# Kernel optimization log

Hardware: AMD Instinct MI355X
Metric: run time of the kernel (lower is better)

The kernel has to match this reference:

```python
import jax, jax.numpy as jnp
import numpy as np

N_ITEMS = 30000
N_HOPS = 2
TMP = 0.2
EPS = 1e-12


def _l2norm(x):
    # F.normalize(x, dim=1): x / max(||x||_2, eps)
    n = jnp.sqrt(jnp.sum(x * x, axis=1, keepdims=True))
    return x / jnp.maximum(n, EPS)


def setup_inputs() -> dict:
    key = jax.random.key(0)
    ks = jax.random.split(key, 12)
    n_users, n_entities, n_items, d = 50000, 100000, N_ITEMS, 64
    n_rel, n_fac, n_cls = 16, 4, 8
    n_edges, n_inter = 1000000, 500000
    return {
        'user_emb': jax.random.normal(ks[0], (n_users, d), jnp.float32),
        'entity_emb': jax.random.normal(ks[1], (n_entities, d), jnp.float32),
        'cls_emb': jax.random.normal(ks[2], (n_cls, d), jnp.float32),
        'latent_emb': jax.random.normal(ks[3], (n_fac, d), jnp.float32),
        'relation_emb': jax.random.normal(ks[4], (n_rel, d), jnp.float32),
        'disen_weight_att': jax.random.normal(ks[5], (n_fac, n_rel), jnp.float32),
        'edge_index': jax.random.randint(ks[6], (2, n_edges), 0, n_entities, jnp.int32),
        'edge_type': jax.random.randint(ks[7], (n_edges,), 0, n_rel, jnp.int32),
        'inter_user': jax.random.randint(ks[8], (n_inter,), 0, n_users, jnp.int32),
        'inter_item': jax.random.randint(ks[9], (n_inter,), 0, n_items, jnp.int32),
        'inter_val': jax.random.uniform(ks[10], (n_inter,), jnp.float32),
        'inter_cls': jax.random.randint(ks[11], (n_inter,), 0, n_cls, jnp.int32),
    }


def _cls_aggregate(entity_emb, user_emb, cls_emb, latent_emb, relation_emb,
                   disen_weight_att, edge_index, edge_type,
                   inter_user, inter_item, inter_val, inter_cls,
                   n_users, n_cls):
    n_entities = entity_emb.shape[0]
    item_emb = entity_emb[:N_ITEMS]
    # --- KG aggregate: scatter_mean over head of entity_emb[tail]*rel[edge_type]
    head, tail = edge_index[0], edge_index[1]
    msg = entity_emb[tail] * relation_emb[edge_type]            # [E, d]
    ent_sum = jax.ops.segment_sum(msg, head, num_segments=n_entities)
    cnt = jax.ops.segment_sum(jnp.ones_like(head, jnp.float32), head,
                              num_segments=n_entities)
    entity_agg = ent_sum / jnp.maximum(cnt, 1.0)[:, None]
    # --- user aggregate: sparse interact_mat @ item_emb
    u_msg = inter_val[:, None] * item_emb[inter_item]           # [I, d]
    user_agg = jax.ops.segment_sum(u_msg, inter_user, num_segments=n_users)
    # --- intent attention
    user_disen_att = jax.nn.softmax(user_emb @ latent_emb.T, axis=1)  # [U, F]
    disen_weight = jax.nn.softmax(disen_weight_att, axis=-1) @ relation_emb  # [F, d]
    user_agg = user_disen_att @ disen_weight + user_agg
    # --- class attention: inter_cls_mat[c] @ item_emb for each class
    user_cls_att = jax.nn.softmax(user_emb @ cls_emb.T, axis=1)  # [U, C]
    seg = inter_cls * n_users + inter_user
    user_cls = jax.ops.segment_sum(u_msg, seg, num_segments=n_cls * n_users)
    user_cls = user_cls.reshape(n_cls, n_users, -1)              # [C, U, d]
    user_agg = jnp.einsum('cud,uc->ud', user_cls, user_cls_att) + user_agg
    return entity_agg, user_agg


def _mutual_information(t, temperature):
    nt = _l2norm(t)
    scores = jnp.exp(nt @ nt.T / temperature)
    return -jnp.sum(jnp.log(jnp.diag(scores) / jnp.sum(scores, axis=1)))


def reference(user_emb, entity_emb, cls_emb, latent_emb, relation_emb,
              disen_weight_att, edge_index, edge_type, inter_user,
              inter_item, inter_val, inter_cls):
    n_users = user_emb.shape[0]
    n_cls = cls_emb.shape[0]
    entity_res, user_res = entity_emb, user_emb
    e, u = entity_emb, user_emb
    for _ in range(N_HOPS):
        e, u = _cls_aggregate(e, u, cls_emb, latent_emb, relation_emb,
                              disen_weight_att, edge_index, edge_type,
                              inter_user, inter_item, inter_val, inter_cls,
                              n_users, n_cls)
        e = _l2norm(e)
        u = _l2norm(u)
        entity_res = entity_res + e
        user_res = user_res + u
    cor_loss = _mutual_information(disen_weight_att, TMP)
    return entity_res, user_res, cor_loss
```

## Files before the change

kernel.cpp:

```cpp
#include <hip/hip_runtime.h>
#include <math.h>

typedef unsigned int uint;

constexpr int N_USERS  = 50000;
constexpr int N_ENT    = 100000;
constexpr int D        = 64;
constexpr int N_FAC    = 4;
constexpr int N_CLS    = 8;
constexpr int N_REL    = 16;
constexpr int N_EDGES  = 1000000;
constexpr int N_INTER  = 500000;

constexpr int BSH      = 7;
constexpr int SPB      = 1 << BSH;
constexpr int NBKT_E   = (N_ENT   + SPB - 1) / SPB;
constexpr int NBKT_U   = (N_USERS + SPB - 1) / SPB;
constexpr int CHUNK    = 4096;
constexpr int NB_E     = (N_EDGES + CHUNK - 1) / CHUNK;
constexpr int NB_U     = (N_INTER + CHUNK - 1) / CHUNK;
constexpr int EBUF_CAP = 3072;

constexpr int E_ROWS   = N_ENT + 1;

constexpr int CVT_BLKS = 2047;

static_assert(NB_E <= 256 && NB_U <= 256, "k_final local scan assumes NB <= 256");

typedef _Float16 h2_t __attribute__((ext_vector_type(2)));
union U32H2 { uint u; h2_t h; };

__device__ inline float h_lo(uint v) { U32H2 x; x.u = v; return (float)x.h.x; }
__device__ inline float h_hi(uint v) { U32H2 x; x.u = v; return (float)x.h.y; }
__device__ inline uint packh(float a, float b) {
    auto r = __builtin_amdgcn_cvt_pkrtz(a, b);
    union { decltype(r) h; uint u; } x;
    x.h = r;
    return x.u;
}

__device__ inline int wscan64_incl(int x, int lane) {
#pragma unroll
    for (int off = 1; off < 64; off <<= 1) {
        int v = __shfl_up(x, off, 64);
        if (lane >= off) x += v;
    }
    return x;
}

__device__ inline int block_scan_incl(int x, int* wsum) {
    int lane = threadIdx.x & 63, wv = threadIdx.x >> 6;
#pragma unroll
    for (int off = 1; off < 64; off <<= 1) {
        int v = __shfl_up(x, off, 64);
        if (lane >= off) x += v;
    }
    if (lane == 63) wsum[wv] = x;
    __syncthreads();
    if (wv == 0 && lane < 16) {
        int s = wsum[lane];
#pragma unroll
        for (int off = 1; off < 16; off <<= 1) {
            int v = __shfl_up(s, off, 64);
            if (lane >= off) s += v;
        }
        wsum[lane] = s;
    }
    __syncthreads();
    if (wv > 0) x += wsum[wv - 1];
    return x;
}

__global__ void k_cvt_dw(const float2* __restrict__ in, uint* __restrict__ out,
                         int n_src, int n_out,
                         const float* __restrict__ datt,
                         const float* __restrict__ rel,
                         float* __restrict__ dw,
                         float* __restrict__ loss_out,
                         uint4* __restrict__ relh4,
                         int* __restrict__ totE,
                         int* __restrict__ totU) {
    __shared__ float p[N_FAC][N_REL];
    __shared__ float nrm[N_FAC];
    __shared__ float sc[N_FAC][N_FAC];
    int t = threadIdx.x;
    int b = blockIdx.x;
    if (b < CVT_BLKS) {
        for (int i = b * 256 + t; i < n_out; i += CVT_BLKS * 256) {
            if (i < n_src) {
                float2 v = in[i];
                out[i] = packh(v.x, v.y);
            } else {
                out[i] = 0u;
            }
        }
        return;
    }
    for (int s = t; s < NBKT_E; s += 256) totE[s] = 0;
    for (int s = t; s < NBKT_U; s += 256) totU[s] = 0;
    for (int s = t; s < N_REL * 8; s += 256) {
        int r = s >> 3, kk = s & 7;
        const float* rp = rel + r * 64 + kk * 8;
        relh4[s] = make_uint4(packh(rp[0], rp[1]), packh(rp[2], rp[3]),
                              packh(rp[4], rp[5]), packh(rp[6], rp[7]));
    }
    if (t < N_FAC) {
        float m = -1e30f;
        for (int r = 0; r < N_REL; ++r) m = fmaxf(m, datt[t * N_REL + r]);
        float tmp[N_REL]; float s = 0.f;
        for (int r = 0; r < N_REL; ++r) { tmp[r] = expf(datt[t * N_REL + r] - m); s += tmp[r]; }
        for (int r = 0; r < N_REL; ++r) p[t][r] = tmp[r] / s;
        float ss = 0.f;
        for (int r = 0; r < N_REL; ++r) { float v = datt[t * N_REL + r]; ss += v * v; }
        nrm[t] = fmaxf(sqrtf(ss), 1e-12f);
    }
    __syncthreads();
    if (t < D) {
        for (int f = 0; f < N_FAC; ++f) {
            float acc = 0.f;
            for (int r = 0; r < N_REL; ++r) acc += p[f][r] * rel[r * D + t];
            dw[f * D + t] = acc;
        }
    }
    if (t < N_FAC * N_FAC) {
        int i = t >> 2, j = t & 3;
        float s = 0.f;
        for (int r = 0; r < N_REL; ++r) s += datt[i * N_REL + r] * datt[j * N_REL + r];
        s /= nrm[i] * nrm[j];
        sc[i][j] = expf(s * 5.0f);
    }
    __syncthreads();
    if (t == 0) {
        float loss = 0.f;
        for (int i = 0; i < N_FAC; ++i) {
            float rowsum = 0.f;
            for (int j = 0; j < N_FAC; ++j) rowsum += sc[i][j];
            loss += logf(sc[i][i] / rowsum);
        }
        *loss_out = -loss;
    }
}

__global__ void k_sort(const int* __restrict__ headE, const int* __restrict__ tailE,
                       const int* __restrict__ etype,
                       const int* __restrict__ iu, const int* __restrict__ ii,
                       const int* __restrict__ icls, const float* __restrict__ ival,
                       uint2* __restrict__ stagE, int* __restrict__ GE, int* __restrict__ RE,
                       uint2* __restrict__ stagU, int* __restrict__ GU, int* __restrict__ RU,
                       int* __restrict__ totE, int* __restrict__ totU) {
    __shared__ int hist[NBKT_E];
    __shared__ int soff[NBKT_E + 1];
    __shared__ int cursor[NBKT_E];
    __shared__ int wsum[16];
    __shared__ uint2 sorted[CHUNK];
    int bid = blockIdx.x;
    bool isE = bid < NB_E;
    int blk  = isE ? bid : bid - NB_E;
    int n    = isE ? N_EDGES : N_INTER;
    int nbkt = isE ? NBKT_E : NBKT_U;
    int base = blk * CHUNK;
    int end  = min(base + CHUNK, n);
    int cblk = end - base;

    for (int b = threadIdx.x; b < nbkt; b += 256) hist[b] = 0;
    __syncthreads();

    uint2 ent[16]; int ebk[16];
#pragma unroll
    for (int j = 0; j < 16; ++j) {
        int i = base + threadIdx.x + j * 256;
        ebk[j] = -1;
        if (i < end) {
            uint x, y; int b;
            if (isE) {
                int h = headE[i];
                x = (uint)h; y = (uint)((tailE[i] << 4) | etype[i]); b = h >> BSH;
            } else {
                int u = iu[i];
                x = (uint)((u << 15) | ii[i]);
                y = (__float_as_uint(ival[i]) & ~7u) | (uint)icls[i];
                b = u >> BSH;
            }
            ent[j] = make_uint2(x, y); ebk[j] = b;
            atomicAdd(&hist[b], 1);
        }
    }
    __syncthreads();

    int b0 = threadIdx.x * 4;
    int lsum[4]; int mysum = 0;
#pragma unroll
    for (int j = 0; j < 4; ++j) {
        int b = b0 + j;
        int v = (b < nbkt) ? hist[b] : 0;
        lsum[j] = mysum; mysum += v;
    }
    int excl = block_scan_incl(mysum, wsum) - mysum;
#pragma unroll
    for (int j = 0; j < 4; ++j) {
        int b = b0 + j;
        if (b < nbkt) soff[b] = excl + lsum[j];
    }
    if (threadIdx.x == 0) soff[nbkt] = cblk;
    __syncthreads();
    for (int b = threadIdx.x; b < nbkt; b += 256) cursor[b] = soff[b];
    __syncthreads();

#pragma unroll
    for (int j = 0; j < 16; ++j) {
        if (ebk[j] >= 0) {
            int p = atomicAdd(&cursor[ebk[j]], 1);
            sorted[p] = ent[j];
        }
    }
    __syncthreads();

    uint2* stag = isE ? stagE : stagU;
    int* G = isE ? GE : GU;
    int* R = isE ? RE : RU;
    int* tot = isE ? totE : totU;
    for (int i = threadIdx.x; i < cblk; i += 256) stag[blk * CHUNK + i] = sorted[i];
    for (int b = threadIdx.x; b < nbkt; b += 256) {
        G[blk * nbkt + b] = hist[b];
        if (hist[b]) atomicAdd(&tot[b], hist[b]);
    }
    for (int b = threadIdx.x; b <= nbkt; b += 256) R[blk * (nbkt + 1) + b] = soff[b];
}

__device__ inline void scan_tot(const int* __restrict__ tot, int* __restrict__ base,
                                int nbkt, int l, int* __restrict__ off_last, int nseg) {
    int carry = 0;
    for (int b = 0; b < nbkt; b += 64) {
        int x = (b + l < nbkt) ? tot[b + l] : 0;
        int incl = wscan64_incl(x, l);
        if (b + l < nbkt) base[b + l] = carry + incl - x;
        carry += __shfl(incl, 63, 64);
    }
    if (l == 0) {
        base[nbkt] = carry;
        off_last[nseg] = carry;
        off_last[nseg + 1] = carry;
    }
}

__global__ void k_base(const int* __restrict__ totE, int* __restrict__ baseE,
                       const int* __restrict__ totU, int* __restrict__ baseU,
                       int* __restrict__ eoff, int* __restrict__ uoff) {
    int t = threadIdx.x;
    if (t < 64) scan_tot(totE, baseE, NBKT_E, t, eoff, N_ENT);
    else        scan_tot(totU, baseU, NBKT_U, t - 64, uoff, N_USERS);
}

__global__ void k_final(const uint2* __restrict__ stagE, const int* __restrict__ GE,
                        const int* __restrict__ RE, const int* __restrict__ baseE,
                        const uint2* __restrict__ stagU, const int* __restrict__ GU,
                        const int* __restrict__ RU, const int* __restrict__ baseU,
                        int* __restrict__ eoff, int* __restrict__ uoff,
                        int* __restrict__ epay, int2* __restrict__ ipv) {
    __shared__ uint2 ebuf[EBUF_CAP];
    __shared__ int cnt[SPB], soff[SPB], cur[SPB];
    __shared__ int wsum[16];
    int bid = blockIdx.x;
    bool isE = bid < NBKT_E;
    int bkt = bid < NBKT_E ? bid : bid - NBKT_E;
    const uint2* stag = isE ? stagE : stagU;
    const int* G  = isE ? GE : GU;
    const int* R  = isE ? RE : RU;
    const int* bb = isE ? baseE : baseU;
    int* off      = isE ? eoff : uoff;
    int NB   = isE ? NB_E : NB_U;
    int nbkt = isE ? NBKT_E : NBKT_U;
    int nseg = isE ? N_ENT : N_USERS;
    int r0 = bb[bkt], r1 = bb[bkt + 1];
    int bsz = r1 - r0;
    int t = threadIdx.x;
    int myc = (t < NB) ? G[t * nbkt + bkt] : 0;
    int mydst = block_scan_incl(myc, wsum) - myc;
    if (t < SPB) cnt[t] = 0;
    if (t < NB) {
        int rs  = R[t * (nbkt + 1) + bkt];
        int re  = R[t * (nbkt + 1) + bkt + 1];
        for (int j = rs; j < re; ++j) {
            int d = mydst + (j - rs);
            if (d < EBUF_CAP) ebuf[d] = stag[t * CHUNK + j];
        }
    }
    __syncthreads();
    for (int i = t; i < bsz; i += 256) {
        uint2 e = ebuf[i];
        int s = (int)(isE ? e.x : (e.x >> 15)) & (SPB - 1);
        atomicAdd(&cnt[s], 1);
    }
    __syncthreads();
    if (t < 64) {
        int a0 = cnt[2 * t], a1 = cnt[2 * t + 1];
        int incl = wscan64_incl(a0 + a1, t);
        int excl = incl - (a0 + a1);
        soff[2 * t] = excl;
        soff[2 * t + 1] = excl + a0;
    }
    __syncthreads();
    if (t < SPB) {
        cur[t] = soff[t];
        int seg = bkt * SPB + t;
        if (seg < nseg) off[seg] = r0 + soff[t];
    }
    __syncthreads();
    for (int i = t; i < bsz; i += 256) {
        uint2 e = ebuf[i];
        int s = (int)(isE ? e.x : (e.x >> 15)) & (SPB - 1);
        int pos = r0 + atomicAdd(&cur[s], 1);
        if (isE) {
            epay[pos] = (int)e.y;
        } else {
            int item = (int)(e.x & 0x7FFF), cls = (int)(e.y & 7u);
            ipv[pos] = make_int2((item << 3) | cls, (int)(e.y & ~7u));
        }
    }
}

template<int MODE>
__global__ __launch_bounds__(256)
void k_hop(const uint4* __restrict__ etab,
           const float4* __restrict__ entbase,
           const float4* __restrict__ usrbase,
           const uint4* __restrict__ ustate_in,
           const uint4* __restrict__ relh4,
           const int* __restrict__ eoff,
           const int* __restrict__ epay,
           const int* __restrict__ uoff,
           const int2* __restrict__ ipv,
           const float4* __restrict__ latent4,
           const float4* __restrict__ cls4,
           const float4* __restrict__ dw4,
           float* __restrict__ att4,
           float* __restrict__ att8,
           uint4* __restrict__ stateE_out,
           uint4* __restrict__ stateU_out,
           float4* __restrict__ outE,
           float4* __restrict__ outU) {
    __shared__ uint4  s_rel[N_REL * 8];
    __shared__ float4 s_dw [N_FAC * 16];
    __shared__ float4 s_lat[N_FAC * 16];
    __shared__ float4 s_cls[N_CLS * 16];
    {
        int t = threadIdx.x;
        if (t < N_REL * 8) s_rel[t] = relh4[t];
        if (t < N_FAC * 16) s_dw[t] = dw4[t];
        if (MODE == 0) {
            if (t < N_FAC * 16) s_lat[t] = latent4[t];
            if (t < N_CLS * 16) s_cls[t] = cls4[t];
        }
    }
    __syncthreads();

    int gid = blockIdx.x * 256 + threadIdx.x;
    int gw = gid >> 3;
    int k = threadIdx.x & 7;
    if (gw >= E_ROWS + N_USERS) return;
    bool isEnt = gw < E_ROWS;
    float a0 = 0.f, a1 = 0.f, a2 = 0.f, a3 = 0.f;
    float a4 = 0.f, a5 = 0.f, a6 = 0.f, a7 = 0.f;

    if (isEnt) {
        int w = gw;
        int beg = eoff[w], end = eoff[w + 1];
        int nE = end - beg;
        const int* pp = epay + beg;
        int pc[8];
#pragma unroll
        for (int q = 0; q < 8; ++q) pc[q] = pp[q];
        for (int bse = 0; bse < nE; bse += 8) {
            int c = nE - bse;
            int pn[8];
#pragma unroll
            for (int q = 0; q < 8; ++q) pn[q] = pp[bse + 8 + q];
            uint4 ev[8], rl[8];
#pragma unroll
            for (int q = 0; q < 8; ++q) {
                int p = (q < c) ? pc[q] : (N_ENT << 4);
                ev[q] = etab[(((size_t)(p >> 4)) << 3) + k];
                rl[q] = s_rel[((p & 15) << 3) + k];
            }
#pragma unroll
            for (int q = 0; q < 8; ++q) {
                a0 = fmaf(h_lo(ev[q].x), h_lo(rl[q].x), a0);
                a1 = fmaf(h_hi(ev[q].x), h_hi(rl[q].x), a1);
                a2 = fmaf(h_lo(ev[q].y), h_lo(rl[q].y), a2);
                a3 = fmaf(h_hi(ev[q].y), h_hi(rl[q].y), a3);
                a4 = fmaf(h_lo(ev[q].z), h_lo(rl[q].z), a4);
                a5 = fmaf(h_hi(ev[q].z), h_hi(rl[q].z), a5);
                a6 = fmaf(h_lo(ev[q].w), h_lo(rl[q].w), a6);
                a7 = fmaf(h_hi(ev[q].w), h_hi(rl[q].w), a7);
            }
#pragma unroll
            for (int q = 0; q < 8; ++q) pc[q] = pn[q];
        }
        float ss = a0*a0 + a1*a1 + a2*a2 + a3*a3 + a4*a4 + a5*a5 + a6*a6 + a7*a7;
#pragma unroll
        for (int m = 1; m < 8; m <<= 1) ss += __shfl_xor(ss, m, 8);
        float s = 1.0f / fmaxf(sqrtf(ss), 1e-12f);
        float v0 = a0*s, v1 = a1*s, v2 = a2*s, v3 = a3*s;
        float v4 = a4*s, v5 = a5*s, v6 = a6*s, v7 = a7*s;
        if (MODE == 0) {
            stateE_out[((size_t)w << 3) + k] =
                make_uint4(packh(v0, v1), packh(v2, v3), packh(v4, v5), packh(v6, v7));
        } else if (w < N_ENT) {
            size_t b = ((size_t)w << 4) + (k << 1);
            float4 b0 = entbase[b], b1 = entbase[b + 1];
            uint4 own = etab[((size_t)w << 3) + k];
            float4 o0 = make_float4(b0.x + h_lo(own.x) + v0, b0.y + h_hi(own.x) + v1,
                                    b0.z + h_lo(own.y) + v2, b0.w + h_hi(own.y) + v3);
            float4 o1 = make_float4(b1.x + h_lo(own.z) + v4, b1.y + h_hi(own.z) + v5,
                                    b1.z + h_lo(own.w) + v6, b1.w + h_hi(own.w) + v7);
            outE[b] = o0; outE[b + 1] = o1;
        }
    } else {
        int w = gw - E_ROWS;
        int beg = uoff[w], end = uoff[w + 1];
        int nE = end - beg;
        const int2* pv = ipv + beg;

        float af0, af1, af2, af3, a8v;
        if (MODE == 0) {
            size_t bb = ((size_t)w << 4) + (k << 1);
            float4 x0 = usrbase[bb], x1 = usrbase[bb + 1];
            float d[12];
#pragma unroll
            for (int f = 0; f < 12; ++f) {
                const float4* lp = (f < 4 ? s_lat + f * 16 : s_cls + (f - 4) * 16) + (k << 1);
                float4 l0 = lp[0], l1 = lp[1];
                d[f] = x0.x*l0.x + x0.y*l0.y + x0.z*l0.z + x0.w*l0.w
                     + x1.x*l1.x + x1.y*l1.y + x1.z*l1.z + x1.w*l1.w;
            }
#pragma unroll
            for (int j = 0; j < 12; ++j) {
#pragma unroll
                for (int off = 1; off < 8; off <<= 1) d[j] += __shfl_xor(d[j], off, 8);
            }
            float m4 = fmaxf(fmaxf(d[0], d[1]), fmaxf(d[2], d[3]));
            float e40 = expf(d[0] - m4), e41 = expf(d[1] - m4);
            float e42 = expf(d[2] - m4), e43 = expf(d[3] - m4);
            float r4 = 1.0f / (e40 + e41 + e42 + e43);
            af0 = e40 * r4; af1 = e41 * r4; af2 = e42 * r4; af3 = e43 * r4;
            float m8 = d[4];
#pragma unroll
            for (int c = 1; c < 8; ++c) m8 = fmaxf(m8, d[4 + c]);
            float e8[8]; float s8 = 0.f;
#pragma unroll
            for (int c = 0; c < 8; ++c) { e8[c] = expf(d[4 + c] - m8); s8 += e8[c]; }
            float a8e = e8[0];
#pragma unroll
            for (int c = 1; c < 8; ++c) if (k == c) a8e = e8[c];
            a8v = a8e / s8;
        } else {
            af0 = att4[w * 4 + 0]; af1 = att4[w * 4 + 1];
            af2 = att4[w * 4 + 2]; af3 = att4[w * 4 + 3];
            a8v = att8[w * 8 + k];
        }

        int2 ec[8];
#pragma unroll
        for (int q = 0; q < 8; ++q) ec[q] = pv[q];
        for (int bse = 0; bse < nE; bse += 8) {
            int c = nE - bse;
            int2 en[8];
#pragma unroll
            for (int q = 0; q < 8; ++q) en[q] = pv[bse + 8 + q];
            uint4 ev[8]; float wg[8];
#pragma unroll
            for (int q = 0; q < 8; ++q) {
                int p = ec[q].x;
                int pe = (q < c) ? p : 0;
                ev[q] = etab[(((size_t)(pe >> 3)) << 3) + k];
                float wgt = __int_as_float(ec[q].y) * (1.0f + __shfl(a8v, p & 7, 8));
                wg[q] = (q < c) ? wgt : 0.0f;
            }
#pragma unroll
            for (int q = 0; q < 8; ++q) {
                a0 = fmaf(h_lo(ev[q].x), wg[q], a0);
                a1 = fmaf(h_hi(ev[q].x), wg[q], a1);
                a2 = fmaf(h_lo(ev[q].y), wg[q], a2);
                a3 = fmaf(h_hi(ev[q].y), wg[q], a3);
                a4 = fmaf(h_lo(ev[q].z), wg[q], a4);
                a5 = fmaf(h_hi(ev[q].z), wg[q], a5);
                a6 = fmaf(h_lo(ev[q].w), wg[q], a6);
                a7 = fmaf(h_hi(ev[q].w), wg[q], a7);
            }
#pragma unroll
            for (int q = 0; q < 8; ++q) ec[q] = en[q];
        }
        {
            const float4* dd0 = s_dw + 0 * 16 + (k << 1);
            const float4* dd1 = s_dw + 1 * 16 + (k << 1);
            const float4* dd2 = s_dw + 2 * 16 + (k << 1);
            const float4* dd3 = s_dw + 3 * 16 + (k << 1);
#pragma unroll
            for (int f = 0; f < 4; ++f) {
                float a = (f == 0) ? af0 : (f == 1) ? af1 : (f == 2) ? af2 : af3;
                const float4* dd = (f == 0) ? dd0 : (f == 1) ? dd1 : (f == 2) ? dd2 : dd3;
                float4 d0 = dd[0], d1 = dd[1];
                a0 = fmaf(a, d0.x, a0); a1 = fmaf(a, d0.y, a1);
                a2 = fmaf(a, d0.z, a2); a3 = fmaf(a, d0.w, a3);
                a4 = fmaf(a, d1.x, a4); a5 = fmaf(a, d1.y, a5);
                a6 = fmaf(a, d1.z, a6); a7 = fmaf(a, d1.w, a7);
            }
        }
        float ss = a0*a0 + a1*a1 + a2*a2 + a3*a3 + a4*a4 + a5*a5 + a6*a6 + a7*a7;
#pragma unroll
        for (int m = 1; m < 8; m <<= 1) ss += __shfl_xor(ss, m, 8);
        float s = 1.0f / fmaxf(sqrtf(ss), 1e-12f);
        float v0 = a0*s, v1 = a1*s, v2 = a2*s, v3 = a3*s;
        float v4 = a4*s, v5 = a5*s, v6 = a6*s, v7 = a7*s;
        if (MODE == 0) {
            stateU_out[((size_t)w << 3) + k] =
                make_uint4(packh(v0, v1), packh(v2, v3), packh(v4, v5), packh(v6, v7));
            float d[12];
#pragma unroll
            for (int f = 0; f < 12; ++f) {
                const float4* lp = (f < 4 ? s_lat + f * 16 : s_cls + (f - 4) * 16) + (k << 1);
                float4 l0 = lp[0], l1 = lp[1];
                d[f] = v0*l0.x + v1*l0.y + v2*l0.z + v3*l0.w
                     + v4*l1.x + v5*l1.y + v6*l1.z + v7*l1.w;
            }
#pragma unroll
            for (int j = 0; j < 12; ++j) {
#pragma unroll
                for (int off = 1; off < 8; off <<= 1) d[j] += __shfl_xor(d[j], off, 8);
            }
            float m4 = fmaxf(fmaxf(d[0], d[1]), fmaxf(d[2], d[3]));
            float e40 = expf(d[0] - m4), e41 = expf(d[1] - m4);
            float e42 = expf(d[2] - m4), e43 = expf(d[3] - m4);
            float r4 = 1.0f / (e40 + e41 + e42 + e43);
            if (k < 4) {
                float v = (k == 0) ? e40 : (k == 1) ? e41 : (k == 2) ? e42 : e43;
                att4[w * 4 + k] = v * r4;
            }
            float m8 = d[4];
#pragma unroll
            for (int c = 1; c < 8; ++c) m8 = fmaxf(m8, d[4 + c]);
            float e8[8]; float s8 = 0.f;
#pragma unroll
            for (int c = 0; c < 8; ++c) { e8[c] = expf(d[4 + c] - m8); s8 += e8[c]; }
            float a8e = e8[0];
#pragma unroll
            for (int c = 1; c < 8; ++c) if (k == c) a8e = e8[c];
            att8[w * 8 + k] = a8e / s8;
        } else {
            uint4 own = ustate_in[((size_t)w << 3) + k];
            size_t b = ((size_t)w << 4) + (k << 1);
            float4 b0 = usrbase[b], b1 = usrbase[b + 1];
            float4 o0 = make_float4(b0.x + h_lo(own.x) + v0, b0.y + h_hi(own.x) + v1,
                                    b0.z + h_lo(own.y) + v2, b0.w + h_hi(own.y) + v3);
            float4 o1 = make_float4(b1.x + h_lo(own.z) + v4, b1.y + h_hi(own.z) + v5,
                                    b1.z + h_lo(own.w) + v6, b1.w + h_hi(own.w) + v7);
            outU[b] = o0; outU[b + 1] = o1;
        }
    }
}

extern "C" void kernel_launch(void* const* d_in, const int* in_sizes, int n_in,
                              void* d_out, int out_size, void* d_ws, size_t ws_size,
                              hipStream_t stream) {
    const float* user_emb   = (const float*)d_in[0];
    const float* entity_emb = (const float*)d_in[1];
    const float* cls_emb    = (const float*)d_in[2];
    const float* latent_emb = (const float*)d_in[3];
    const float* rel_emb    = (const float*)d_in[4];
    const float* disen      = (const float*)d_in[5];
    const int*   edge_index = (const int*)d_in[6];
    const int*   edge_type  = (const int*)d_in[7];
    const int*   inter_user = (const int*)d_in[8];
    const int*   inter_item = (const int*)d_in[9];
    const float* inter_val  = (const float*)d_in[10];
    const int*   inter_cls  = (const int*)d_in[11];

    float* out      = (float*)d_out;
    float* out_ent  = out;
    float* out_user = out + (size_t)N_ENT * D;
    float* out_loss = out + (size_t)N_ENT * D + (size_t)N_USERS * D;

    char* w = (char*)d_ws;
    auto alloc = [&](size_t bytes) -> char* {
        char* p = w;
        w += (bytes + 255) & ~(size_t)255;
        return p;
    };
    uint*  ebuf0 = (uint*)alloc((size_t)E_ROWS * 32 * 4);
    uint*  eA    = (uint*)alloc((size_t)E_ROWS * 32 * 4);
    uint*  uA    = (uint*)alloc((size_t)N_USERS * 32 * 4);
    int*   epay  = (int*)alloc((size_t)(N_EDGES + 32) * 4);
    int2*  ipv   = (int2*)alloc((size_t)(N_INTER + 32) * 8);
    int*   eoff  = (int*)alloc((size_t)(N_ENT + 4) * 4);
    int*   uoff  = (int*)alloc((size_t)(N_USERS + 4) * 4);
    int*   GE    = (int*)alloc((size_t)NB_E * NBKT_E * 4);
    int*   RE    = (int*)alloc((size_t)NB_E * (NBKT_E + 1) * 4);
    int*   GU    = (int*)alloc((size_t)NB_U * NBKT_U * 4);
    int*   RU    = (int*)alloc((size_t)NB_U * (NBKT_U + 1) * 4);
    int*   totE  = (int*)alloc((size_t)NBKT_E * 4);
    int*   totU  = (int*)alloc((size_t)NBKT_U * 4);
    int*   baseE = (int*)alloc((size_t)(NBKT_E + 1) * 4);
    int*   baseU = (int*)alloc((size_t)(NBKT_U + 1) * 4);
    uint4* relh  = (uint4*)alloc((size_t)N_REL * 8 * 16);
    float* dw    = (float*)alloc((size_t)N_FAC * D * 4);
    float* att4  = (float*)alloc((size_t)N_USERS * N_FAC * 4);
    float* att8  = (float*)alloc((size_t)N_USERS * N_CLS * 4);

    uint2* stagE = (uint2*)eA;
    uint2* stagU = (uint2*)uA;

    const int* head = edge_index;
    const int* tail = edge_index + N_EDGES;

    k_cvt_dw<<<CVT_BLKS + 1, 256, 0, stream>>>(
        (const float2*)entity_emb, ebuf0, N_ENT * 32, E_ROWS * 32,
        disen, rel_emb, dw, out_loss, relh, totE, totU);
    k_sort <<<NB_E + NB_U, 256, 0, stream>>>(head, tail, edge_type,
                                             inter_user, inter_item, inter_cls, inter_val,
                                             stagE, GE, RE, stagU, GU, RU, totE, totU);
    k_base <<<1, 128, 0, stream>>>(totE, baseE, totU, baseU, eoff, uoff);
    k_final<<<NBKT_E + NBKT_U, 256, 0, stream>>>(stagE, GE, RE, baseE,
                                                 stagU, GU, RU, baseU,
                                                 eoff, uoff, epay, ipv);

    const int hop_blocks = ((E_ROWS + N_USERS) * 8 + 255) / 256;

    k_hop<0><<<hop_blocks, 256, 0, stream>>>((const uint4*)ebuf0, nullptr,
                                             (const float4*)user_emb, nullptr,
                                             relh, eoff, epay, uoff, ipv,
                                             (const float4*)latent_emb,
                                             (const float4*)cls_emb,
                                             (const float4*)dw,
                                             att4, att8,
                                             (uint4*)eA, (uint4*)uA,
                                             nullptr, nullptr);

    k_hop<1><<<hop_blocks, 256, 0, stream>>>((const uint4*)eA,
                                             (const float4*)entity_emb,
                                             (const float4*)user_emb,
                                             (const uint4*)uA,
                                             relh, eoff, epay, uoff, ipv,
                                             (const float4*)latent_emb,
                                             (const float4*)cls_emb,
                                             (const float4*)dw,
                                             att4, att8,
                                             nullptr, nullptr,
                                             (float4*)out_ent, (float4*)out_user);
}
```

Measured before the change: 132.3 us.

## Fuse convert and sort kernels, fold bucket-base scan into final pass

Merges the fp16 conversion/dw-loss kernel with the bucket-sort kernel into one launch, so both run concurrently in disjoint block ranges. The single-block k_base scan kernel is removed: each k_final block now computes its own bucket base with a parallel reduction over the preceding bucket totals, and the last bucket writes the offsets sentinel. Bucket totals are zeroed with memsets instead of inside the kernel. This drops kernel launches and a serial dependency point, at the cost of redundant per-block prefix reductions in k_final.

```diff
diff --git a/kernel.cpp b/kernel.cpp
--- a/kernel.cpp
+++ b/kernel.cpp
@@ -23,7 +23,8 @@
 
 constexpr int E_ROWS   = N_ENT + 1;
 
-constexpr int CVT_BLKS = 2047;
+constexpr int SORT_BLKS = NB_E + NB_U;
+constexpr int CVT2_BLKS = 2048;
 
 static_assert(NB_E <= 256 && NB_U <= 256, "k_final local scan assumes NB <= 256");
 
@@ -71,89 +72,87 @@
     return x;
 }
 
-__global__ void k_cvt_dw(const float2* __restrict__ in, uint* __restrict__ out,
-                         int n_src, int n_out,
-                         const float* __restrict__ datt,
-                         const float* __restrict__ rel,
-                         float* __restrict__ dw,
-                         float* __restrict__ loss_out,
-                         uint4* __restrict__ relh4,
-                         int* __restrict__ totE,
-                         int* __restrict__ totU) {
-    __shared__ float p[N_FAC][N_REL];
-    __shared__ float nrm[N_FAC];
-    __shared__ float sc[N_FAC][N_FAC];
+__global__ void k_sortcvt(const int* __restrict__ headE, const int* __restrict__ tailE,
+                          const int* __restrict__ etype,
+                          const int* __restrict__ iu, const int* __restrict__ ii,
+                          const int* __restrict__ icls, const float* __restrict__ ival,
+                          uint2* __restrict__ stagE, int* __restrict__ GE, int* __restrict__ RE,
+                          uint2* __restrict__ stagU, int* __restrict__ GU, int* __restrict__ RU,
+                          int* __restrict__ totE, int* __restrict__ totU,
+                          const float2* __restrict__ cin, uint* __restrict__ cout,
+                          int n_src, int n_out,
+                          const float* __restrict__ datt,
+                          const float* __restrict__ rel,
+                          float* __restrict__ dw,
+                          float* __restrict__ loss_out,
+                          uint4* __restrict__ relh4) {
+    int bid = blockIdx.x;
     int t = threadIdx.x;
-    int b = blockIdx.x;
-    if (b < CVT_BLKS) {
-        for (int i = b * 256 + t; i < n_out; i += CVT_BLKS * 256) {
-            if (i < n_src) {
-                float2 v = in[i];
-                out[i] = packh(v.x, v.y);
-            } else {
-                out[i] = 0u;
-            }
+    if (bid >= SORT_BLKS) {
+        int cb = bid - SORT_BLKS;
+        if (cb < CVT2_BLKS) {
+            for (int i = cb * 256 + t; i < n_out; i += CVT2_BLKS * 256) {
+                if (i < n_src) {
+                    float2 v = cin[i];
+                    cout[i] = packh(v.x, v.y);
+                } else {
+                    cout[i] = 0u;
+                }
+            }
+            return;
+        }
+        __shared__ float p[N_FAC][N_REL];
+        __shared__ float nrm[N_FAC];
+        __shared__ float sc[N_FAC][N_FAC];
+        for (int s = t; s < N_REL * 8; s += 256) {
+            int r = s >> 3, kk = s & 7;
+            const float* rp = rel + r * 64 + kk * 8;
+            relh4[s] = make_uint4(packh(rp[0], rp[1]), packh(rp[2], rp[3]),
+                                  packh(rp[4], rp[5]), packh(rp[6], rp[7]));
+        }
+        if (t < N_FAC) {
+            float m = -1e30f;
+            for (int r = 0; r < N_REL; ++r) m = fmaxf(m, datt[t * N_REL + r]);
+            float tmp[N_REL]; float s = 0.f;
+            for (int r = 0; r < N_REL; ++r) { tmp[r] = expf(datt[t * N_REL + r] - m); s += tmp[r]; }
+            for (int r = 0; r < N_REL; ++r) p[t][r] = tmp[r] / s;
+            float ss = 0.f;
+            for (int r = 0; r < N_REL; ++r) { float v = datt[t * N_REL + r]; ss += v * v; }
+            nrm[t] = fmaxf(sqrtf(ss), 1e-12f);
+        }
+        __syncthreads();
+        if (t < D) {
+            for (int f = 0; f < N_FAC; ++f) {
+                float acc = 0.f;
+                for (int r = 0; r < N_REL; ++r) acc += p[f][r] * rel[r * D + t];
+                dw[f * D + t] = acc;
+            }
+        }
+        if (t < N_FAC * N_FAC) {
+            int i = t >> 2, j = t & 3;
+            float s = 0.f;
+            for (int r = 0; r < N_REL; ++r) s += datt[i * N_REL + r] * datt[j * N_REL + r];
+            s /= nrm[i] * nrm[j];
+            sc[i][j] = expf(s * 5.0f);
+        }
+        __syncthreads();
+        if (t == 0) {
+            float loss = 0.f;
+            for (int i = 0; i < N_FAC; ++i) {
+                float rowsum = 0.f;
+                for (int j = 0; j < N_FAC; ++j) rowsum += sc[i][j];
+                loss += logf(sc[i][i] / rowsum);
+            }
+            *loss_out = -loss;
         }
         return;
     }
-    for (int s = t; s < NBKT_E; s += 256) totE[s] = 0;
-    for (int s = t; s < NBKT_U; s += 256) totU[s] = 0;
-    for (int s = t; s < N_REL * 8; s += 256) {
-        int r = s >> 3, kk = s & 7;
-        const float* rp = rel + r * 64 + kk * 8;
-        relh4[s] = make_uint4(packh(rp[0], rp[1]), packh(rp[2], rp[3]),
-                              packh(rp[4], rp[5]), packh(rp[6], rp[7]));
-    }
-    if (t < N_FAC) {
-        float m = -1e30f;
-        for (int r = 0; r < N_REL; ++r) m = fmaxf(m, datt[t * N_REL + r]);
-        float tmp[N_REL]; float s = 0.f;
-        for (int r = 0; r < N_REL; ++r) { tmp[r] = expf(datt[t * N_REL + r] - m); s += tmp[r]; }
-        for (int r = 0; r < N_REL; ++r) p[t][r] = tmp[r] / s;
-        float ss = 0.f;
-        for (int r = 0; r < N_REL; ++r) { float v = datt[t * N_REL + r]; ss += v * v; }
-        nrm[t] = fmaxf(sqrtf(ss), 1e-12f);
-    }
-    __syncthreads();
-    if (t < D) {
-        for (int f = 0; f < N_FAC; ++f) {
-            float acc = 0.f;
-            for (int r = 0; r < N_REL; ++r) acc += p[f][r] * rel[r * D + t];
-            dw[f * D + t] = acc;
-        }
-    }
-    if (t < N_FAC * N_FAC) {
-        int i = t >> 2, j = t & 3;
-        float s = 0.f;
-        for (int r = 0; r < N_REL; ++r) s += datt[i * N_REL + r] * datt[j * N_REL + r];
-        s /= nrm[i] * nrm[j];
-        sc[i][j] = expf(s * 5.0f);
-    }
-    __syncthreads();
-    if (t == 0) {
-        float loss = 0.f;
-        for (int i = 0; i < N_FAC; ++i) {
-            float rowsum = 0.f;
-            for (int j = 0; j < N_FAC; ++j) rowsum += sc[i][j];
-            loss += logf(sc[i][i] / rowsum);
-        }
-        *loss_out = -loss;
-    }
-}
-
-__global__ void k_sort(const int* __restrict__ headE, const int* __restrict__ tailE,
-                       const int* __restrict__ etype,
-                       const int* __restrict__ iu, const int* __restrict__ ii,
-                       const int* __restrict__ icls, const float* __restrict__ ival,
-                       uint2* __restrict__ stagE, int* __restrict__ GE, int* __restrict__ RE,
-                       uint2* __restrict__ stagU, int* __restrict__ GU, int* __restrict__ RU,
-                       int* __restrict__ totE, int* __restrict__ totU) {
+
     __shared__ int hist[NBKT_E];
     __shared__ int soff[NBKT_E + 1];
     __shared__ int cursor[NBKT_E];
     __shared__ int wsum[16];
     __shared__ uint2 sorted[CHUNK];
-    int bid = blockIdx.x;
     bool isE = bid < NB_E;
     int blk  = isE ? bid : bid - NB_E;
     int n    = isE ? N_EDGES : N_INTER;
@@ -162,13 +161,13 @@
     int end  = min(base + CHUNK, n);
     int cblk = end - base;
 
-    for (int b = threadIdx.x; b < nbkt; b += 256) hist[b] = 0;
+    for (int b = t; b < nbkt; b += 256) hist[b] = 0;
     __syncthreads();
 
     uint2 ent[16]; int ebk[16];
 #pragma unroll
     for (int j = 0; j < 16; ++j) {
-        int i = base + threadIdx.x + j * 256;
+        int i = base + t + j * 256;
         ebk[j] = -1;
         if (i < end) {
             uint x, y; int b;
@@ -187,7 +186,7 @@
     }
     __syncthreads();
 
-    int b0 = threadIdx.x * 4;
+    int b0 = t * 4;
     int lsum[4]; int mysum = 0;
 #pragma unroll
     for (int j = 0; j < 4; ++j) {
@@ -201,9 +200,9 @@
         int b = b0 + j;
         if (b < nbkt) soff[b] = excl + lsum[j];
     }
-    if (threadIdx.x == 0) soff[nbkt] = cblk;
-    __syncthreads();
-    for (int b = threadIdx.x; b < nbkt; b += 256) cursor[b] = soff[b];
+    if (t == 0) soff[nbkt] = cblk;
+    __syncthreads();
+    for (int b = t; b < nbkt; b += 256) cursor[b] = soff[b];
     __syncthreads();
 
 #pragma unroll
@@ -219,42 +218,18 @@
     int* G = isE ? GE : GU;
     int* R = isE ? RE : RU;
     int* tot = isE ? totE : totU;
-    for (int i = threadIdx.x; i < cblk; i += 256) stag[blk * CHUNK + i] = sorted[i];
-    for (int b = threadIdx.x; b < nbkt; b += 256) {
+    for (int i = t; i < cblk; i += 256) stag[blk * CHUNK + i] = sorted[i];
+    for (int b = t; b < nbkt; b += 256) {
         G[blk * nbkt + b] = hist[b];
         if (hist[b]) atomicAdd(&tot[b], hist[b]);
     }
-    for (int b = threadIdx.x; b <= nbkt; b += 256) R[blk * (nbkt + 1) + b] = soff[b];
+    for (int b = t; b <= nbkt; b += 256) R[blk * (nbkt + 1) + b] = soff[b];
 }
 
-__device__ inline void scan_tot(const int* __restrict__ tot, int* __restrict__ base,
-                                int nbkt, int l, int* __restrict__ off_last, int nseg) {
-    int carry = 0;
-    for (int b = 0; b < nbkt; b += 64) {
-        int x = (b + l < nbkt) ? tot[b + l] : 0;
-        int incl = wscan64_incl(x, l);
-        if (b + l < nbkt) base[b + l] = carry + incl - x;
-        carry += __shfl(incl, 63, 64);
-    }
-    if (l == 0) {
-        base[nbkt] = carry;
-        off_last[nseg] = carry;
-        off_last[nseg + 1] = carry;
-    }
-}
-
-__global__ void k_base(const int* __restrict__ totE, int* __restrict__ baseE,
-                       const int* __restrict__ totU, int* __restrict__ baseU,
-                       int* __restrict__ eoff, int* __restrict__ uoff) {
-    int t = threadIdx.x;
-    if (t < 64) scan_tot(totE, baseE, NBKT_E, t, eoff, N_ENT);
-    else        scan_tot(totU, baseU, NBKT_U, t - 64, uoff, N_USERS);
-}
-
 __global__ void k_final(const uint2* __restrict__ stagE, const int* __restrict__ GE,
-                        const int* __restrict__ RE, const int* __restrict__ baseE,
+                        const int* __restrict__ RE, const int* __restrict__ totE,
                         const uint2* __restrict__ stagU, const int* __restrict__ GU,
-                        const int* __restrict__ RU, const int* __restrict__ baseU,
+                        const int* __restrict__ RU, const int* __restrict__ totU,
                         int* __restrict__ eoff, int* __restrict__ uoff,
                         int* __restrict__ epay, int2* __restrict__ ipv) {
     __shared__ uint2 ebuf[EBUF_CAP];
@@ -262,20 +237,31 @@
     __shared__ int wsum[16];
     int bid = blockIdx.x;
     bool isE = bid < NBKT_E;
-    int bkt = bid < NBKT_E ? bid : bid - NBKT_E;
+    int bkt = isE ? bid : bid - NBKT_E;
     const uint2* stag = isE ? stagE : stagU;
     const int* G  = isE ? GE : GU;
     const int* R  = isE ? RE : RU;
-    const int* bb = isE ? baseE : baseU;
+    const int* tot = isE ? totE : totU;
     int* off      = isE ? eoff : uoff;
     int NB   = isE ? NB_E : NB_U;
     int nbkt = isE ? NBKT_E : NBKT_U;
     int nseg = isE ? N_ENT : N_USERS;
-    int r0 = bb[bkt], r1 = bb[bkt + 1];
-    int bsz = r1 - r0;
     int t = threadIdx.x;
+    int lane = t & 63, wv = t >> 6;
+
+    int part = 0;
+    for (int b = t; b < bkt; b += 256) part += tot[b];
+#pragma unroll
+    for (int off_ = 1; off_ < 64; off_ <<= 1) part += __shfl_xor(part, off_, 64);
+    if (lane == 0) wsum[wv] = part;
+    __syncthreads();
+    int r0 = wsum[0] + wsum[1] + wsum[2] + wsum[3];
+    int r1 = r0 + tot[bkt];
+    __syncthreads();
+
     int myc = (t < NB) ? G[t * nbkt + bkt] : 0;
     int mydst = block_scan_incl(myc, wsum) - myc;
+    int bsz = r1 - r0;
     if (t < SPB) cnt[t] = 0;
     if (t < NB) {
         int rs  = R[t * (nbkt + 1) + bkt];
@@ -284,6 +270,10 @@
             int d = mydst + (j - rs);
             if (d < EBUF_CAP) ebuf[d] = stag[t * CHUNK + j];
         }
+    }
+    if (t == 0 && bkt == nbkt - 1) {
+        off[nseg] = r1;
+        if (isE) off[nseg + 1] = r1;
     }
     __syncthreads();
     for (int i = t; i < bsz; i += 256) {
@@ -491,14 +481,10 @@
             for (int q = 0; q < 8; ++q) ec[q] = en[q];
         }
         {
-            const float4* dd0 = s_dw + 0 * 16 + (k << 1);
-            const float4* dd1 = s_dw + 1 * 16 + (k << 1);
-            const float4* dd2 = s_dw + 2 * 16 + (k << 1);
-            const float4* dd3 = s_dw + 3 * 16 + (k << 1);
 #pragma unroll
             for (int f = 0; f < 4; ++f) {
                 float a = (f == 0) ? af0 : (f == 1) ? af1 : (f == 2) ? af2 : af3;
-                const float4* dd = (f == 0) ? dd0 : (f == 1) ? dd1 : (f == 2) ? dd2 : dd3;
+                const float4* dd = s_dw + f * 16 + (k << 1);
                 float4 d0 = dd[0], d1 = dd[1];
                 a0 = fmaf(a, d0.x, a0); a1 = fmaf(a, d0.y, a1);
                 a2 = fmaf(a, d0.z, a2); a3 = fmaf(a, d0.w, a3);
@@ -599,8 +585,6 @@
     int*   RU    = (int*)alloc((size_t)NB_U * (NBKT_U + 1) * 4);
     int*   totE  = (int*)alloc((size_t)NBKT_E * 4);
     int*   totU  = (int*)alloc((size_t)NBKT_U * 4);
-    int*   baseE = (int*)alloc((size_t)(NBKT_E + 1) * 4);
-    int*   baseU = (int*)alloc((size_t)(NBKT_U + 1) * 4);
     uint4* relh  = (uint4*)alloc((size_t)N_REL * 8 * 16);
     float* dw    = (float*)alloc((size_t)N_FAC * D * 4);
     float* att4  = (float*)alloc((size_t)N_USERS * N_FAC * 4);
@@ -612,15 +596,17 @@
     const int* head = edge_index;
     const int* tail = edge_index + N_EDGES;
 
-    k_cvt_dw<<<CVT_BLKS + 1, 256, 0, stream>>>(
+    hipMemsetAsync(totE, 0, (size_t)NBKT_E * 4, stream);
+    hipMemsetAsync(totU, 0, (size_t)NBKT_U * 4, stream);
+
+    k_sortcvt<<<SORT_BLKS + CVT2_BLKS + 1, 256, 0, stream>>>(
+        head, tail, edge_type, inter_user, inter_item, inter_cls, inter_val,
+        stagE, GE, RE, stagU, GU, RU, totE, totU,
         (const float2*)entity_emb, ebuf0, N_ENT * 32, E_ROWS * 32,
-        disen, rel_emb, dw, out_loss, relh, totE, totU);
-    k_sort <<<NB_E + NB_U, 256, 0, stream>>>(head, tail, edge_type,
-                                             inter_user, inter_item, inter_cls, inter_val,
-                                             stagE, GE, RE, stagU, GU, RU, totE, totU);
-    k_base <<<1, 128, 0, stream>>>(totE, baseE, totU, baseU, eoff, uoff);
-    k_final<<<NBKT_E + NBKT_U, 256, 0, stream>>>(stagE, GE, RE, baseE,
-                                                 stagU, GU, RU, baseU,
+        disen, rel_emb, dw, out_loss, relh);
+
+    k_final<<<NBKT_E + NBKT_U, 256, 0, stream>>>(stagE, GE, RE, totE,
+                                                 stagU, GU, RU, totU,
                                                  eoff, uoff, epay, ipv);
 
     const int hop_blocks = ((E_ROWS + N_USERS) * 8 + 255) / 256;
```

Result: no change. 134.1 us (+1.3%).
